# Optimization experiments

Hardware: AMD Instinct MI355X
Metric: run time of the kernel (lower is better)

Reference implementation:

```python
import jax, jax.numpy as jnp
import numpy as np

N_NODES = 50000
N_EDGES = 100000
N_GRAPHS = 2000
F_IN = 32      # num_node_features
EF = 16        # num_edge_features (unpacked bits)
H = 32         # hidden_dim
H2 = 64        # hidden_dim * 2


def _lin(key, fan_in, fan_out):
    kw, kb = jax.random.split(key)
    scale = 1.0 / np.sqrt(fan_in)
    W = jax.random.uniform(kw, (fan_in, fan_out), jnp.float32, -scale, scale)
    b = jax.random.uniform(kb, (fan_out,), jnp.float32, -scale, scale)
    return W, b


def setup_inputs() -> dict:
    key = jax.random.key(0)
    ks = jax.random.split(key, 16)
    x = jax.random.normal(ks[0], (N_NODES, F_IN), jnp.float32)
    edge_index = jax.random.randint(ks[1], (2, N_EDGES), 0, N_NODES, jnp.int64)
    edge_attr_packed = jax.random.randint(ks[2], (N_EDGES, 2), 0, 256, jnp.int32)
    batch = jnp.sort(jax.random.randint(ks[3], (N_NODES,), 0, N_GRAPHS, jnp.int64))

    W1a, b1a = _lin(ks[4], EF, H * F_IN)
    W1b, b1b = _lin(ks[5], H * F_IN, H * F_IN)
    W2a, b2a = _lin(ks[6], EF, H * H)
    W2b, b2b = _lin(ks[7], H * H, H * H * 2)
    root1 = jax.random.normal(ks[8], (F_IN, H), jnp.float32) / np.sqrt(F_IN)
    bias1 = jnp.zeros((H,), jnp.float32)
    root2 = jax.random.normal(ks[9], (H, H2), jnp.float32) / np.sqrt(H)
    bias2 = jnp.zeros((H2,), jnp.float32)
    fcW1, fcb1 = _lin(ks[10], H2, 512)
    fcW2, fcb2 = _lin(ks[11], 512, 512)
    fcW3, fcb3 = _lin(ks[12], 512, 256)
    fcW4, fcb4 = _lin(ks[13], 256, 3)
    return dict(x=x, edge_index=edge_index, edge_attr_packed=edge_attr_packed, batch=batch,
                W1a=W1a, b1a=b1a, W1b=W1b, b1b=b1b, W2a=W2a, b2a=b2a, W2b=W2b, b2b=b2b,
                root1=root1, bias1=bias1, root2=root2, bias2=bias2,
                fcW1=fcW1, fcb1=fcb1, fcW2=fcW2, fcb2=fcb2,
                fcW3=fcW3, fcb3=fcb3, fcW4=fcW4, fcb4=fcb4)


def _unpack_bits(ea_packed):
    # MSB-first bit unpack of each byte, matching torch f_unpackbits(mask=1)
    shifts = jnp.arange(7, -1, -1, dtype=jnp.int32)          # [8]
    bits = (ea_packed[:, :, None] >> shifts) & 1             # [E, W, 8]
    return bits.reshape(ea_packed.shape[0], -1).astype(jnp.float32)  # [E, W*8]


def _seg_mean(vals, idx, n):
    s = jax.ops.segment_sum(vals, idx, num_segments=n)
    c = jax.ops.segment_sum(jnp.ones((vals.shape[0], 1), vals.dtype), idx, num_segments=n)
    return s / jnp.maximum(c, 1.0)


def _nnconv(x, src, dst, theta, root, bias, f_in, f_out):
    # theta: [E, f_in*f_out] -> per-edge weight matrices (PyG view(-1, in, out))
    Wm = theta.reshape(-1, f_in, f_out)
    msg = jnp.einsum('ei,eio->eo', x[src], Wm)               # per-edge matmul
    agg = _seg_mean(msg, dst, x.shape[0])                    # scatter-mean at targets
    return agg + x @ root + bias


def reference(x, edge_index, edge_attr_packed, batch,
              W1a, b1a, W1b, b1b, W2a, b2a, W2b, b2b,
              root1, bias1, root2, bias2,
              fcW1, fcb1, fcW2, fcb2, fcW3, fcb3, fcW4, fcb4):
    relu = jax.nn.relu
    ea = _unpack_bits(edge_attr_packed)                      # [E, 16]
    src, dst = edge_index[0], edge_index[1]

    theta1 = relu(ea @ W1a + b1a) @ W1b + b1b                # [E, H*F_IN]
    h = relu(_nnconv(x, src, dst, theta1, root1, bias1, F_IN, H))

    theta2 = relu(ea @ W2a + b2a) @ W2b + b2b                # [E, H*H2]
    h = relu(_nnconv(h, src, dst, theta2, root2, bias2, H, H2))

    g = _seg_mean(h, batch, N_GRAPHS)                        # global_mean_pool
    g = relu(g @ fcW1 + fcb1)
    g = relu(g @ fcW2 + fcb2)
    g = relu(g @ fcW3 + fcb3)
    return g @ fcW4 + fcb4
```

## Files before the change

### kernel.cpp

```cpp
#include <hip/hip_runtime.h>

#define E_N 100000
#define NV_N 50000
#define NG_N 2000
#define EP 100096
#define NTILES 391

typedef short s8v __attribute__((ext_vector_type(8)));
typedef unsigned short u16x8 __attribute__((ext_vector_type(8)));
typedef unsigned int u32x4 __attribute__((ext_vector_type(4)));
typedef float f32x4 __attribute__((ext_vector_type(4)));

__device__ __forceinline__ float bf2f(unsigned short u) {
  return __uint_as_float(((unsigned int)u) << 16);
}
__device__ __forceinline__ unsigned short f2bf(float f) {
  unsigned int u = __float_as_uint(f);
  u = u + 0x7fffu + ((u >> 16) & 1u);
  return (unsigned short)(u >> 16);
}


__global__ void k_tables(const float* __restrict__ W1a, const float* __restrict__ b1a,
                         const float* __restrict__ W2a, const float* __restrict__ b2a,
                         unsigned short* __restrict__ tabs) {
  int tid = blockIdx.x * 256 + threadIdx.x;
  int tb = tid >> 18, v = (tid >> 10) & 255, k = tid & 1023;
  const float* W = (tb < 2) ? W1a : W2a;
  int rbase = (tb & 1) ? 8 : 0;
  float s = 0.f;
  if ((tb & 1) == 0) s = (tb < 2) ? b1a[k] : b2a[k];
  #pragma unroll
  for (int j = 0; j < 8; ++j)
    if ((v >> (7 - j)) & 1) s += W[(rbase + j) * 1024 + k];
  tabs[tid] = f2bf(s);
}

__global__ void k_pack(const float* __restrict__ src, unsigned short* __restrict__ dst, int N) {
  int tid = blockIdx.x * 256 + threadIdx.x;
  int total = (1024 / 8) * N;
  if (tid >= total) return;
  int fi = tid >> 6, r = tid & 63;
  int lg = r >> 4, ll = r & 15;
  int nf = fi & 1, ks = (fi >> 1) & 1;
  int rest = fi >> 2;
  int nc32 = N / 32;
  int cb = rest % nc32, q = rest / nc32;
  int k0 = q * 64 + ks * 32 + lg * 8;
  int n = cb * 32 + nf * 16 + ll;
  u16x8 v;
  #pragma unroll
  for (int u = 0; u < 8; ++u)
    v[u] = f2bf(src[(size_t)(k0 + u) * N + n]);
  *(u16x8*)&dst[(size_t)tid * 8] = v;
}

__global__ void k_count(const int* __restrict__ ei, int* __restrict__ cnt) {
  int e = blockIdx.x * 256 + threadIdx.x;
  if (e < E_N) atomicAdd(&cnt[ei[E_N + e]], 1);
}

template<int NCOLS, int FOUT>
__global__ void __launch_bounds__(256, 2)
k_edge(const float* __restrict__ xsrc, const int* __restrict__ ei,
       const int* __restrict__ eap,
       const unsigned short* __restrict__ tab0,
       const unsigned short* __restrict__ tab1,
       const unsigned short* __restrict__ WP,
       const float* __restrict__ bvec,
       float* __restrict__ agg)
{
  constexpr int NP = NCOLS / 64;

  __shared__ unsigned short sHid[256 * 64];
  __shared__ float sXT[32 * 264];
  __shared__ int sSrc[256], sDst[256];
  __shared__ unsigned char sb0[256], sb1[256];

  const int t = threadIdx.x;
  const int l = t & 63;
  const int wid = t >> 6;
  const int wr = wid >> 1;
  const int wc = wid & 1;
  const int lg = l >> 4;
  const int ll = l & 15;

  const int part = blockIdx.x / NTILES;
  const int tile = blockIdx.x - part * NTILES;
  const int q0 = (part == 0) ? 0 : (part == 1 ? 6 : 11);
  const int q1 = (part == 0) ? 6 : (part == 1 ? 11 : 16);
  const int e0 = tile * 256;

  auto build = [&](int q) {
    const unsigned short* p0 = tab0 + (size_t)sb0[t] * 1024 + q * 64;
    const unsigned short* p1 = tab1 + (size_t)sb1[t] * 1024 + q * 64;
    #pragma unroll
    for (int j = 0; j < 8; ++j) {
      u16x8 a = *(const u16x8*)(p0 + j * 8);
      u16x8 b = *(const u16x8*)(p1 + j * 8);
      u32x4 hw;
      #pragma unroll
      for (int p = 0; p < 4; ++p) {
        float f0 = fmaxf(bf2f(a[2 * p]) + bf2f(b[2 * p]), 0.f);
        float f1 = fmaxf(bf2f(a[2 * p + 1]) + bf2f(b[2 * p + 1]), 0.f);
        unsigned int r01;
        asm("v_cvt_pk_bf16_f32 %0, %1, %2" : "=v"(r01) : "v"(f0), "v"(f1));
        hw[p] = r01;
      }
      *(u32x4*)&sHid[t * 64 + 8 * (j ^ (t & 7))] = hw;
    }
  };

  const unsigned short* bp = WP + (size_t)q0 * (NCOLS / 32) * 2048
                                + (size_t)wc * 2048 + (size_t)l * 8;
  s8v rb[2][2];
  rb[0][0] = *(const s8v*)bp;
  rb[0][1] = *(const s8v*)(bp + 512);
  rb[1][0] = *(const s8v*)(bp + 1024);
  rb[1][1] = *(const s8v*)(bp + 1536);
  bp += 4096;

  {
    int e = e0 + t;
    if (e < E_N) {
      sSrc[t] = ei[e]; sDst[t] = ei[E_N + e];
      sb0[t] = (unsigned char)(eap[2 * e] & 255);
      sb1[t] = (unsigned char)(eap[2 * e + 1] & 255);
    } else { sSrc[t] = 0; sDst[t] = -1; sb0[t] = 0; sb1[t] = 0; }
  }
  __syncthreads();
  for (int j = t; j < 256 * 32; j += 256) {
    int m = j >> 5, i = j & 31;
    sXT[i * 264 + m] = (e0 + m < E_N) ? xsrc[(size_t)sSrc[m] * 32 + i] : 0.f;
  }
  build(q0);
  __syncthreads();

  f32x4 msgr[2][4][2] = {};

  #pragma unroll 1
  for (int q = q0; q < q1; ++q) {
    if (q > q0) {
      __syncthreads();
      build(q);
      __syncthreads();
    }
    s8v av[2][4][2];
    #pragma unroll
    for (int hf = 0; hf < 2; ++hf)
      #pragma unroll
      for (int mf = 0; mf < 4; ++mf) {
        int row = hf * 128 + wr * 64 + mf * 16 + ll;
        #pragma unroll
        for (int ks = 0; ks < 2; ++ks) {
          int kb = ks * 4 + lg;
          av[hf][mf][ks] = *(const s8v*)&sHid[row * 64 + 8 * (kb ^ (row & 7))];
          asm volatile("" : "+v"(av[hf][mf][ks]));
        }
      }
    #pragma unroll 1
    for (int np = 0; np < NP; ++np) {
      const int iidx = (FOUT == 64) ? np : np * 2 + wc;
      f32x4 acc[4][2];
      f32x4 xv[4];
      #pragma unroll
      for (int mf = 0; mf < 4; ++mf)
        xv[mf] = *(const f32x4*)&sXT[iidx * 264 + wr * 64 + mf * 16 + lg * 4];
      __builtin_amdgcn_s_setprio(1);
      #pragma unroll
      for (int mf = 0; mf < 4; ++mf)
        #pragma unroll
        for (int nf = 0; nf < 2; ++nf)
          acc[mf][nf] = __builtin_amdgcn_mfma_f32_16x16x32_bf16(
              av[0][mf][0], rb[0][nf], (f32x4){0.f, 0.f, 0.f, 0.f}, 0, 0, 0);
      #pragma unroll
      for (int mf = 0; mf < 4; ++mf)
        #pragma unroll
        for (int nf = 0; nf < 2; ++nf)
          acc[mf][nf] = __builtin_amdgcn_mfma_f32_16x16x32_bf16(
              av[0][mf][1], rb[1][nf], acc[mf][nf], 0, 0, 0);
      __builtin_amdgcn_s_setprio(0);
      #pragma unroll
      for (int mf = 0; mf < 4; ++mf) {
        msgr[0][mf][0] += acc[mf][0] * xv[mf];
        msgr[0][mf][1] += acc[mf][1] * xv[mf];
      }
      #pragma unroll
      for (int mf = 0; mf < 4; ++mf)
        xv[mf] = *(const f32x4*)&sXT[iidx * 264 + 128 + wr * 64 + mf * 16 + lg * 4];
      __builtin_amdgcn_s_setprio(1);
      #pragma unroll
      for (int mf = 0; mf < 4; ++mf)
        #pragma unroll
        for (int nf = 0; nf < 2; ++nf)
          acc[mf][nf] = __builtin_amdgcn_mfma_f32_16x16x32_bf16(
              av[1][mf][0], rb[0][nf], (f32x4){0.f, 0.f, 0.f, 0.f}, 0, 0, 0);
      __builtin_amdgcn_s_setprio(0);
      rb[0][0] = *(const s8v*)bp;
      rb[0][1] = *(const s8v*)(bp + 512);
      __builtin_amdgcn_s_setprio(1);
      #pragma unroll
      for (int mf = 0; mf < 4; ++mf)
        #pragma unroll
        for (int nf = 0; nf < 2; ++nf)
          acc[mf][nf] = __builtin_amdgcn_mfma_f32_16x16x32_bf16(
              av[1][mf][1], rb[1][nf], acc[mf][nf], 0, 0, 0);
      __builtin_amdgcn_s_setprio(0);
      rb[1][0] = *(const s8v*)(bp + 1024);
      rb[1][1] = *(const s8v*)(bp + 1536);
      bp += 4096;
      #pragma unroll
      for (int mf = 0; mf < 4; ++mf) {
        msgr[1][mf][0] += acc[mf][0] * xv[mf];
        msgr[1][mf][1] += acc[mf][1] * xv[mf];
      }
    }
  }

  if (part == 0) {
    #pragma unroll 4
    for (int i = 0; i < 32; ++i) {
      if (FOUT == 32 && (i & 1) != wc) continue;
      float w0, w1;
      {
        int ob = (FOUT == 64) ? wc * 32 : 0;
        w0 = bvec[i * FOUT + ob + ll];
        w1 = bvec[i * FOUT + ob + 16 + ll];
      }
      #pragma unroll
      for (int hf = 0; hf < 2; ++hf)
        #pragma unroll
        for (int mf = 0; mf < 4; ++mf) {
          f32x4 xv = *(const f32x4*)&sXT[i * 264 + hf * 128 + wr * 64 + mf * 16 + lg * 4];
          msgr[hf][mf][0] += xv * w0;
          msgr[hf][mf][1] += xv * w1;
        }
    }
  }

  #pragma unroll
  for (int hf = 0; hf < 2; ++hf)
    #pragma unroll
    for (int nf = 0; nf < 2; ++nf) {
      const int o = ((FOUT == 64) ? (wc * 2 + nf) * 16 : nf * 16) + ll;
      #pragma unroll
      for (int mf = 0; mf < 4; ++mf)
        #pragma unroll
        for (int r = 0; r < 4; ++r) {
          int row = hf * 128 + wr * 64 + mf * 16 + lg * 4 + r;
          int d = sDst[row];
          if (d >= 0) atomicAdd(&agg[(size_t)d * FOUT + o], msgr[hf][mf][nf][r]);
        }
    }
}


__global__ void k_node1(const float* __restrict__ x, const float* __restrict__ agg,
                        const int* __restrict__ cnt, const float* __restrict__ root,
                        const float* __restrict__ bias, float* __restrict__ h) {
  int tid = blockIdx.x * 256 + threadIdx.x;
  if (tid >= NV_N * 32) return;
  int n = tid >> 5, j = tid & 31;
  const float* xr = x + n * 32;
  float s = 0.f;
  #pragma unroll
  for (int i = 0; i < 32; ++i) s = fmaf(xr[i], root[i * 32 + j], s);
  int c = cnt[n]; if (c < 1) c = 1;
  h[tid] = fmaxf(agg[tid] / (float)c + s + bias[j], 0.f);
}

__global__ void k_node2(const float* __restrict__ hin, const float* __restrict__ agg,
                        const int* __restrict__ cnt, const float* __restrict__ root,
                        const float* __restrict__ bias, float* __restrict__ h2) {
  int tid = blockIdx.x * 256 + threadIdx.x;
  if (tid >= NV_N * 64) return;
  int n = tid >> 6, j = tid & 63;
  const float* xr = hin + n * 32;
  float s = 0.f;
  #pragma unroll
  for (int i = 0; i < 32; ++i) s = fmaf(xr[i], root[i * 64 + j], s);
  int c = cnt[n]; if (c < 1) c = 1;
  h2[tid] = fmaxf(agg[tid] / (float)c + s + bias[j], 0.f);
}

__device__ __forceinline__ int lowerb(const int* __restrict__ a, int n, int key) {
  int lo = 0, hi = n;
  while (lo < hi) { int mid = (lo + hi) >> 1; if (a[mid] < key) lo = mid + 1; else hi = mid; }
  return lo;
}

__global__ void k_pool(const float* __restrict__ h2, const int* __restrict__ batch,
                       float* __restrict__ g) {
  int gid = (blockIdx.x * 256 + threadIdx.x) >> 6;
  int l = threadIdx.x & 63;
  if (gid >= NG_N) return;
  int lo = lowerb(batch, NV_N, gid);
  int hi = lowerb(batch, NV_N, gid + 1);
  float s = 0.f;
  for (int n = lo; n < hi; ++n) s += h2[n * 64 + l];
  int c = hi - lo; if (c < 1) c = 1;
  g[gid * 64 + l] = s / (float)c;
}

template<int K, bool RELU>
__global__ void k_fc(const float* __restrict__ A, const float* __restrict__ W,
                     const float* __restrict__ bias, float* __restrict__ out, int N) {
  __shared__ float sA[8][K];
  int r0 = blockIdx.x * 8;
  int n = blockIdx.y * 256 + threadIdx.x;
  for (int j = threadIdx.x; j < 8 * K; j += 256) {
    int rr = j / K, kk = j - rr * K;
    int r = r0 + rr;
    sA[rr][kk] = (r < NG_N) ? A[r * K + kk] : 0.f;
  }
  __syncthreads();
  float acc[8] = {0.f, 0.f, 0.f, 0.f, 0.f, 0.f, 0.f, 0.f};
  for (int k = 0; k < K; ++k) {
    float b = W[k * N + n];
    #pragma unroll
    for (int rr = 0; rr < 8; ++rr) acc[rr] = fmaf(sA[rr][k], b, acc[rr]);
  }
  float bs = bias[n];
  #pragma unroll
  for (int rr = 0; rr < 8; ++rr) {
    int r = r0 + rr;
    if (r < NG_N) {
      float v = acc[rr] + bs;
      if (RELU) v = fmaxf(v, 0.f);
      out[r * N + n] = v;
    }
  }
}

__global__ void k_fc4(const float* __restrict__ A, const float* __restrict__ W,
                      const float* __restrict__ bias, float* __restrict__ out) {
  int tid = blockIdx.x * 256 + threadIdx.x;
  int r = tid >> 2, s = tid & 3;
  if (r >= NG_N || s >= 3) return;
  float acc = bias[s];
  for (int k = 0; k < 256; ++k) acc = fmaf(A[r * 256 + k], W[k * 3 + s], acc);
  out[r * 3 + s] = acc;
}


extern "C" void kernel_launch(void* const* d_in, const int* in_sizes, int n_in,
                              void* d_out, int out_size, void* d_ws, size_t ws_size,
                              hipStream_t stream) {
  const float* x     = (const float*)d_in[0];
  const int*   ei    = (const int*)d_in[1];
  const int*   eap   = (const int*)d_in[2];
  const int*   batch = (const int*)d_in[3];
  const float* W1a   = (const float*)d_in[4];
  const float* b1a   = (const float*)d_in[5];
  const float* W1b   = (const float*)d_in[6];
  const float* b1b   = (const float*)d_in[7];
  const float* W2a   = (const float*)d_in[8];
  const float* b2a   = (const float*)d_in[9];
  const float* W2b   = (const float*)d_in[10];
  const float* b2b   = (const float*)d_in[11];
  const float* root1 = (const float*)d_in[12];
  const float* bias1 = (const float*)d_in[13];
  const float* root2 = (const float*)d_in[14];
  const float* bias2 = (const float*)d_in[15];
  const float* fcW1  = (const float*)d_in[16];
  const float* fcb1  = (const float*)d_in[17];
  const float* fcW2  = (const float*)d_in[18];
  const float* fcb2  = (const float*)d_in[19];
  const float* fcW3  = (const float*)d_in[20];
  const float* fcb3  = (const float*)d_in[21];
  const float* fcW4  = (const float*)d_in[22];
  const float* fcb4  = (const float*)d_in[23];
  float* out = (float*)d_out;

  char* w = (char*)d_ws;
  size_t off = 0;
  auto take = [&](size_t bytes) -> void* {
    void* p = w + off;
    off = (off + bytes + 255) & ~(size_t)255;
    return p;
  };
  unsigned short* tabs = (unsigned short*)take(4 * 256 * 1024 * 2);
  unsigned short* w1p  = (unsigned short*)take((size_t)1024 * 1024 * 2 + 65536);
  unsigned short* w2p  = (unsigned short*)take((size_t)1024 * 2048 * 2 + 65536);
  float* agg1 = (float*)take((size_t)NV_N * 32 * 4);
  float* agg2 = (float*)take((size_t)NV_N * 64 * 4);
  int*   cnt  = (int*)take((size_t)NV_N * 4);
  float* h    = (float*)take((size_t)NV_N * 32 * 4);
  float* h2   = (float*)take((size_t)NV_N * 64 * 4);
  float* g    = (float*)take((size_t)NG_N * 64 * 4);
  float* l1   = (float*)take((size_t)NG_N * 512 * 4);
  float* l2   = (float*)take((size_t)NG_N * 512 * 4);
  float* l3   = (float*)take((size_t)NG_N * 256 * 4);

  hipMemsetAsync(agg1, 0, (size_t)NV_N * 32 * 4, stream);
  hipMemsetAsync(agg2, 0, (size_t)NV_N * 64 * 4, stream);
  hipMemsetAsync(cnt, 0, (size_t)NV_N * 4, stream);

  k_tables<<<4096, 256, 0, stream>>>(W1a, b1a, W2a, b2a, tabs);
  k_pack<<<(1024 * 1024 / 8 + 255) / 256, 256, 0, stream>>>(W1b, w1p, 1024);
  k_pack<<<(1024 * 2048 / 8 + 255) / 256, 256, 0, stream>>>(W2b, w2p, 2048);
  k_count<<<(E_N + 255) / 256, 256, 0, stream>>>(ei, cnt);

  const int nblk = 3 * NTILES;
  k_edge<1024, 32><<<nblk, 256, 0, stream>>>(x, ei, eap, tabs, tabs + 262144,
                                             w1p, b1b, agg1);
  k_node1<<<(NV_N * 32) / 256, 256, 0, stream>>>(x, agg1, cnt, root1, bias1, h);

  k_edge<2048, 64><<<nblk, 256, 0, stream>>>(h, ei, eap, tabs + 2 * 262144, tabs + 3 * 262144,
                                             w2p, b2b, agg2);
  k_node2<<<(NV_N * 64) / 256, 256, 0, stream>>>(h, agg2, cnt, root2, bias2, h2);

  k_pool<<<(NG_N * 64) / 256, 256, 0, stream>>>(h2, batch, g);

  k_fc<64, true><<<dim3((NG_N + 7) / 8, 2), 256, 0, stream>>>(g, fcW1, fcb1, l1, 512);
  k_fc<512, true><<<dim3((NG_N + 7) / 8, 2), 256, 0, stream>>>(l1, fcW2, fcb2, l2, 512);
  k_fc<512, true><<<dim3((NG_N + 7) / 8, 1), 256, 0, stream>>>(l2, fcW3, fcb3, l3, 256);
  k_fc4<<<(NG_N * 4 + 255) / 256, 256, 0, stream>>>(l3, fcW4, fcb4, out);
}
```

Measured before the change: 794.9 us.

## Double-buffer B fragments and software-pipeline MFMA epilogue across iterations

Splits the B-fragment registers into two buffers (rbA/rbB) so weight loads for the next np step are issued a full iteration ahead. It also defers the second half-tile's multiply-accumulate into msgr until the next step's MFMAs have been issued, overlapping VALU and LDS work with matrix instructions. The cost is higher VGPR pressure from the extra accumulators and buffers, which could reduce occupancy. The loop is unrolled by two, so NP is assumed to be even.

```diff
diff --git a/kernel.cpp b/kernel.cpp
--- a/kernel.cpp
+++ b/kernel.cpp
@@ -113,12 +113,16 @@
 
   const unsigned short* bp = WP + (size_t)q0 * (NCOLS / 32) * 2048
                                 + (size_t)wc * 2048 + (size_t)l * 8;
-  s8v rb[2][2];
-  rb[0][0] = *(const s8v*)bp;
-  rb[0][1] = *(const s8v*)(bp + 512);
-  rb[1][0] = *(const s8v*)(bp + 1024);
-  rb[1][1] = *(const s8v*)(bp + 1536);
-  bp += 4096;
+  s8v rbA[2][2], rbB[2][2];
+  rbA[0][0] = *(const s8v*)bp;
+  rbA[0][1] = *(const s8v*)(bp + 512);
+  rbA[1][0] = *(const s8v*)(bp + 1024);
+  rbA[1][1] = *(const s8v*)(bp + 1536);
+  rbB[0][0] = *(const s8v*)(bp + 4096);
+  rbB[0][1] = *(const s8v*)(bp + 4608);
+  rbB[1][0] = *(const s8v*)(bp + 5120);
+  rbB[1][1] = *(const s8v*)(bp + 5632);
+  bp += 8192;
 
   {
     int e = e0 + t;
@@ -137,6 +141,66 @@
   __syncthreads();
 
   f32x4 msgr[2][4][2] = {};
+  f32x4 accA[4][2], accB[4][2];
+  #pragma unroll
+  for (int mf = 0; mf < 4; ++mf)
+    #pragma unroll
+    for (int nf = 0; nf < 2; ++nf)
+      accB[mf][nf] = (f32x4){0.f, 0.f, 0.f, 0.f};
+  int pidx = 0;
+
+  s8v av[2][4][2];
+
+#define NPBODY(RB, NPIDX)                                                     \
+  {                                                                           \
+    const int iidx = (FOUT == 64) ? (NPIDX) : (NPIDX) * 2 + wc;               \
+    __builtin_amdgcn_s_setprio(1);                                            \
+    _Pragma("unroll")                                                         \
+    for (int mf = 0; mf < 4; ++mf)                                            \
+      _Pragma("unroll")                                                       \
+      for (int nf = 0; nf < 2; ++nf)                                          \
+        accA[mf][nf] = __builtin_amdgcn_mfma_f32_16x16x32_bf16(               \
+            av[0][mf][0], RB[0][nf], (f32x4){0.f, 0.f, 0.f, 0.f}, 0, 0, 0);   \
+    _Pragma("unroll")                                                         \
+    for (int mf = 0; mf < 4; ++mf)                                            \
+      _Pragma("unroll")                                                       \
+      for (int nf = 0; nf < 2; ++nf)                                          \
+        accA[mf][nf] = __builtin_amdgcn_mfma_f32_16x16x32_bf16(               \
+            av[0][mf][1], RB[1][nf], accA[mf][nf], 0, 0, 0);                  \
+    __builtin_amdgcn_s_setprio(0);                                            \
+    _Pragma("unroll")                                                         \
+    for (int mf = 0; mf < 4; ++mf) {                                          \
+      f32x4 xv = *(const f32x4*)&sXT[pidx * 264 + 128 + wr * 64 + mf * 16 + lg * 4]; \
+      msgr[1][mf][0] += accB[mf][0] * xv;                                     \
+      msgr[1][mf][1] += accB[mf][1] * xv;                                     \
+    }                                                                         \
+    __builtin_amdgcn_s_setprio(1);                                            \
+    _Pragma("unroll")                                                         \
+    for (int mf = 0; mf < 4; ++mf)                                            \
+      _Pragma("unroll")                                                       \
+      for (int nf = 0; nf < 2; ++nf)                                          \
+        accB[mf][nf] = __builtin_amdgcn_mfma_f32_16x16x32_bf16(               \
+            av[1][mf][0], RB[0][nf], (f32x4){0.f, 0.f, 0.f, 0.f}, 0, 0, 0);   \
+    _Pragma("unroll")                                                         \
+    for (int mf = 0; mf < 4; ++mf)                                            \
+      _Pragma("unroll")                                                       \
+      for (int nf = 0; nf < 2; ++nf)                                          \
+        accB[mf][nf] = __builtin_amdgcn_mfma_f32_16x16x32_bf16(               \
+            av[1][mf][1], RB[1][nf], accB[mf][nf], 0, 0, 0);                  \
+    __builtin_amdgcn_s_setprio(0);                                            \
+    RB[0][0] = *(const s8v*)bp;                                               \
+    RB[0][1] = *(const s8v*)(bp + 512);                                       \
+    RB[1][0] = *(const s8v*)(bp + 1024);                                      \
+    RB[1][1] = *(const s8v*)(bp + 1536);                                      \
+    bp += 4096;                                                               \
+    _Pragma("unroll")                                                         \
+    for (int mf = 0; mf < 4; ++mf) {                                          \
+      f32x4 xv = *(const f32x4*)&sXT[iidx * 264 + wr * 64 + mf * 16 + lg * 4];\
+      msgr[0][mf][0] += accA[mf][0] * xv;                                     \
+      msgr[0][mf][1] += accA[mf][1] * xv;                                     \
+    }                                                                         \
+    pidx = iidx;                                                              \
+  }
 
   #pragma unroll 1
   for (int q = q0; q < q1; ++q) {
@@ -145,7 +209,6 @@
       build(q);
       __syncthreads();
     }
-    s8v av[2][4][2];
     #pragma unroll
     for (int hf = 0; hf < 2; ++hf)
       #pragma unroll
@@ -159,62 +222,18 @@
         }
       }
     #pragma unroll 1
-    for (int np = 0; np < NP; ++np) {
-      const int iidx = (FOUT == 64) ? np : np * 2 + wc;
-      f32x4 acc[4][2];
-      f32x4 xv[4];
-      #pragma unroll
-      for (int mf = 0; mf < 4; ++mf)
-        xv[mf] = *(const f32x4*)&sXT[iidx * 264 + wr * 64 + mf * 16 + lg * 4];
-      __builtin_amdgcn_s_setprio(1);
-      #pragma unroll
-      for (int mf = 0; mf < 4; ++mf)
-        #pragma unroll
-        for (int nf = 0; nf < 2; ++nf)
-          acc[mf][nf] = __builtin_amdgcn_mfma_f32_16x16x32_bf16(
-              av[0][mf][0], rb[0][nf], (f32x4){0.f, 0.f, 0.f, 0.f}, 0, 0, 0);
-      #pragma unroll
-      for (int mf = 0; mf < 4; ++mf)
-        #pragma unroll
-        for (int nf = 0; nf < 2; ++nf)
-          acc[mf][nf] = __builtin_amdgcn_mfma_f32_16x16x32_bf16(
-              av[0][mf][1], rb[1][nf], acc[mf][nf], 0, 0, 0);
-      __builtin_amdgcn_s_setprio(0);
-      #pragma unroll
-      for (int mf = 0; mf < 4; ++mf) {
-        msgr[0][mf][0] += acc[mf][0] * xv[mf];
-        msgr[0][mf][1] += acc[mf][1] * xv[mf];
-      }
-      #pragma unroll
-      for (int mf = 0; mf < 4; ++mf)
-        xv[mf] = *(const f32x4*)&sXT[iidx * 264 + 128 + wr * 64 + mf * 16 + lg * 4];
-      __builtin_amdgcn_s_setprio(1);
-      #pragma unroll
-      for (int mf = 0; mf < 4; ++mf)
-        #pragma unroll
-        for (int nf = 0; nf < 2; ++nf)
-          acc[mf][nf] = __builtin_amdgcn_mfma_f32_16x16x32_bf16(
-              av[1][mf][0], rb[0][nf], (f32x4){0.f, 0.f, 0.f, 0.f}, 0, 0, 0);
-      __builtin_amdgcn_s_setprio(0);
-      rb[0][0] = *(const s8v*)bp;
-      rb[0][1] = *(const s8v*)(bp + 512);
-      __builtin_amdgcn_s_setprio(1);
-      #pragma unroll
-      for (int mf = 0; mf < 4; ++mf)
-        #pragma unroll
-        for (int nf = 0; nf < 2; ++nf)
-          acc[mf][nf] = __builtin_amdgcn_mfma_f32_16x16x32_bf16(
-              av[1][mf][1], rb[1][nf], acc[mf][nf], 0, 0, 0);
-      __builtin_amdgcn_s_setprio(0);
-      rb[1][0] = *(const s8v*)(bp + 1024);
-      rb[1][1] = *(const s8v*)(bp + 1536);
-      bp += 4096;
-      #pragma unroll
-      for (int mf = 0; mf < 4; ++mf) {
-        msgr[1][mf][0] += acc[mf][0] * xv[mf];
-        msgr[1][mf][1] += acc[mf][1] * xv[mf];
-      }
-    }
+    for (int npb = 0; npb < NP; npb += 2) {
+      NPBODY(rbA, npb);
+      NPBODY(rbB, npb + 1);
+    }
+  }
+#undef NPBODY
+
+  #pragma unroll
+  for (int mf = 0; mf < 4; ++mf) {
+    f32x4 xv = *(const f32x4*)&sXT[pidx * 264 + 128 + wr * 64 + mf * 16 + lg * 4];
+    msgr[1][mf][0] += accB[mf][0] * xv;
+    msgr[1][mf][1] += accB[mf][1] * xv;
   }
 
   if (part == 0) {
```

Result: slower. 901.5 us (+13.4%).
